# Kernel tuning notes

Hardware: AMD Instinct MI355X
Metric: run time of the kernel (lower is better)

## Reference

```python
import jax, jax.numpy as jnp
import numpy as np

B, N, D = 4, 2048, 1024

def setup_inputs() -> dict:
    key = jax.random.key(0)
    ks = jax.random.split(key, 8)
    s = 1.0 / np.sqrt(D)
    return {
        "x": jax.random.normal(ks[0], (B, N, D), dtype=jnp.float32),
        "Wq": jax.random.normal(ks[1], (D, D), dtype=jnp.float32) * s,
        "bq": jnp.zeros((D,), dtype=jnp.float32),
        "Wk": jax.random.normal(ks[2], (D, D), dtype=jnp.float32) * s,
        "bk": jnp.zeros((D,), dtype=jnp.float32),
        "Wv": jax.random.normal(ks[3], (D, D), dtype=jnp.float32) * s,
        "bv": jnp.zeros((D,), dtype=jnp.float32),
        "gamma": jnp.ones((1,), dtype=jnp.float32),
    }

def reference(x, Wq, bq, Wk, bk, Wv, bv, gamma):
    d = x.shape[-1]
    delta = 1.0 / jnp.sqrt(jnp.asarray(d, dtype=x.dtype))
    # torch Linear: y = x @ W.T + b, W is [out, in]
    Q = jnp.einsum('bnd,ed->bne', x, Wq) + bq
    K = jnp.einsum('bnd,ed->bne', x, Wk) + bk
    V = jnp.einsum('bnd,ed->bne', x, Wv) + bv
    scores = jnp.einsum('bne,bme->bnm', Q, K) * delta  # [B, N, N]
    attn = jax.nn.softmax(scores, axis=-1)
    out = jnp.einsum('bnm,bme->bne', attn, V)
    return out * gamma + x
```

## Files before the change

### kernel.cpp

```cpp
#include <hip/hip_runtime.h>

typedef _Float16 f16;
typedef __attribute__((ext_vector_type(4))) _Float16 f16x4;
typedef __attribute__((ext_vector_type(8))) _Float16 f16x8;
typedef __attribute__((ext_vector_type(4))) float f32x4;

#define B_ 4
#define N_ 2048
#define D_ 1024

#define FENCE asm volatile("" ::: "memory")

__global__ __launch_bounds__(256) void k_cast_all(const float4* __restrict__ x,
                                                  const float4* __restrict__ wq,
                                                  const float4* __restrict__ wk,
                                                  const float4* __restrict__ wv,
                                                  f16x4* __restrict__ xo,
                                                  f16x4* __restrict__ wqo,
                                                  f16x4* __restrict__ wko,
                                                  f16x4* __restrict__ wvo,
                                                  float* __restrict__ rowsum) {
  int b = blockIdx.x;
  if (b >= 11264) {
    rowsum[(b - 11264) * 256 + threadIdx.x] = 0.f;
    return;
  }
  const float4* in;
  f16x4* out;
  int idx;
  if (b < 8192)       { in = x;  out = xo;  idx = b * 256 + threadIdx.x; }
  else if (b < 9216)  { in = wq; out = wqo; idx = (b - 8192) * 256 + threadIdx.x; }
  else if (b < 10240) { in = wk; out = wko; idx = (b - 9216) * 256 + threadIdx.x; }
  else                { in = wv; out = wvo; idx = (b - 10240) * 256 + threadIdx.x; }
  float4 v = in[idx];
  f16x4 o = { (_Float16)v.x, (_Float16)v.y, (_Float16)v.z, (_Float16)v.w };
  out[idx] = o;
}

__device__ __forceinline__ void stage_half(const char* g0, int ldB, int kByte,
                                           char* slot, int tid) {
#pragma unroll
  for (int r = 0; r < 2; ++r) {
    int lin = r * 8192 + tid * 16;
    int row = lin >> 7;
    int lch = ((lin >> 4) & 7) ^ (row & 7);
    const char* g = g0 + (long)row * ldB + kByte + lch * 16;
    char* l = slot + r * 8192 + ((tid >> 6) << 10);
    __builtin_amdgcn_global_load_lds(
        (const __attribute__((address_space(1))) unsigned int*)g,
        (__attribute__((address_space(3))) unsigned int*)l, 16, 0, 0);
  }
}

#define RD_A(dst, base)                                                          \
  _Pragma("unroll") for (int i_ = 0; i_ < 4; ++i_) {                             \
    int rA_ = wm * 64 + i_ * 16 + l16;                                           \
    _Pragma("unroll") for (int k_ = 0; k_ < 2; ++k_)                             \
      dst[i_][k_] = *(const f16x8*)((base) + rA_ * 128 +                         \
                                    ((((k_ << 2) | quad) ^ l7) << 4));           \
  }
#define RD_B(dst, base)                                                          \
  _Pragma("unroll") for (int j_ = 0; j_ < 2; ++j_) {                             \
    int rB_ = wn * 32 + j_ * 16 + l16;                                           \
    _Pragma("unroll") for (int k_ = 0; k_ < 2; ++k_)                             \
      dst[j_][k_] = *(const f16x8*)((base) + rB_ * 128 +                         \
                                    ((((k_ << 2) | quad) ^ l7) << 4));           \
  }
#define MFMA8(Av, Bv, BH)                                                        \
  __builtin_amdgcn_s_setprio(1);                                                 \
  _Pragma("unroll") for (int i_ = 0; i_ < 4; ++i_)                               \
  _Pragma("unroll") for (int j_ = 0; j_ < 2; ++j_)                               \
  _Pragma("unroll") for (int k_ = 0; k_ < 2; ++k_)                               \
    acc[i_][BH][j_] = __builtin_amdgcn_mfma_f32_16x16x32_f16(                    \
        Av[i_][k_], Bv[j_][k_], acc[i_][BH][j_], 0, 0, 0);                       \
  __builtin_amdgcn_s_setprio(0);

#define D128_TILE(AC, B0C, AN, B0N, q) {                                         \
  char* Sc = lds + (q) * 49152;                                                  \
  char* Sn = lds + ((q) ^ 1) * 49152;                                            \
  const int kB = (t + 1) << 7;                                                   \
           \
  stage_half(gA, ldaB, kB, Sn, tid);                                             \
  stage_half(gB, ldbB, kB, Sn + 16384, tid);                                     \
  asm volatile("s_waitcnt vmcnt(4)" ::: "memory");                               \
  __builtin_amdgcn_s_barrier(); FENCE;                                           \
  RD_B(b1, Sc + 32768);                                                          \
  MFMA8(AC, B0C, 0);                                                             \
                         \
  stage_half(gB1, ldbB, kB, Sn + 32768, tid);                                    \
  asm volatile("s_waitcnt vmcnt(2)" ::: "memory");                               \
  __builtin_amdgcn_s_barrier(); FENCE;                                           \
  RD_A(AN, Sn); RD_B(B0N, Sn + 16384);                                           \
  MFMA8(AC, b1, 1);                                                              \
}
#define D128_TAIL(AC, B0C, q) {                                                  \
  char* Sc = lds + (q) * 49152;                                                  \
  asm volatile("s_waitcnt vmcnt(0)" ::: "memory");                               \
  __builtin_amdgcn_s_barrier(); FENCE;                                           \
  RD_B(b1, Sc + 32768);                                                          \
  MFMA8(AC, B0C, 0);                                                             \
  MFMA8(AC, b1, 1);                                                              \
}

__device__ __forceinline__ void gemm_d128(const char* gA, int ldaB,
                                          const char* gB, int ldbB,
                                          int nK, char* lds, f32x4 acc[4][2][2]) {
  const int tid = threadIdx.x;
  const int lane = tid & 63, wave = tid >> 6;
  const int wm = wave >> 2, wn = wave & 3;
  const int quad = lane >> 4, l16 = lane & 15;
  const int l7 = l16 & 7;
  const char* gB1 = gB + (long)128 * ldbB;
  f16x8 aX[4][2], aY[4][2], b0X[2][2], b0Y[2][2], b1[2][2];
  stage_half(gA,  ldaB, 0, lds, tid);
  stage_half(gB,  ldbB, 0, lds + 16384, tid);
  stage_half(gB1, ldbB, 0, lds + 32768, tid);
  asm volatile("s_waitcnt vmcnt(2)" ::: "memory");
  __builtin_amdgcn_s_barrier(); FENCE;
  RD_A(aX, lds); RD_B(b0X, lds + 16384);
  for (int tb = 0; tb < nK - 2; tb += 2) {
    { const int t = tb;     D128_TILE(aX, b0X, aY, b0Y, 0) }
    { const int t = tb + 1; D128_TILE(aY, b0Y, aX, b0X, 1) }
  }
  { const int t = nK - 2;   D128_TILE(aX, b0X, aY, b0Y, 0) }
  D128_TAIL(aY, b0Y, 1)
  __builtin_amdgcn_s_barrier(); FENCE;
}

__device__ __forceinline__ void gemm256(const char* gA, int ldaB,
                                        const char* gB, int ldbB,
                                        int nK, char* lds, f32x4 acc[2][4][2][2]) {
  const int tid = threadIdx.x;
  const int lane = tid & 63;
  const int wave = tid >> 6;
  const int wm = wave >> 2, wn = wave & 3;
  const int quad = lane >> 4, l16 = lane & 15;
  const int l7 = l16 & 7;
  const char* gA1 = gA + (long)128 * ldaB;
  const char* gB1 = gB + (long)128 * ldbB;
  char* Abuf = lds;
  char* Bbuf = lds + 65536;
  stage_half(gA,  ldaB, 0, Abuf, tid);
  stage_half(gB,  ldbB, 0, Bbuf, tid);
  stage_half(gA1, ldaB, 0, Abuf + 16384, tid);
  stage_half(gB1, ldbB, 0, Bbuf + 16384, tid);
  for (int t = 0; t < nK; ++t) {
    const int c = t & 1;
    char* Ac = Abuf + c * 32768;
    char* Bc = Bbuf + c * 32768;
    char* An = Abuf + (c ^ 1) * 32768;
    char* Bn = Bbuf + (c ^ 1) * 32768;
    const bool st = (t + 1 < nK);
    const int kB = (t + 1) << 7;
    f16x8 afc[2][4][2];
    f16x8 bf[2][2];
#pragma unroll
    for (int ph = 0; ph < 4; ++ph) {
      const int Ah = ph & 1, Bh = ph >> 1;
      if (ph == 0)      { asm volatile("s_waitcnt vmcnt(4)" ::: "memory"); }
      else if (ph == 1) { if (st) asm volatile("s_waitcnt vmcnt(4)" ::: "memory");
                          else    asm volatile("s_waitcnt vmcnt(2)" ::: "memory"); }
      else if (ph == 2) { if (st) asm volatile("s_waitcnt vmcnt(4)" ::: "memory");
                          else    asm volatile("s_waitcnt vmcnt(0)" ::: "memory"); }
      __builtin_amdgcn_s_barrier();
      FENCE;
      if (ph < 2) {
        const char* Ab = Ac + ph * 16384;
#pragma unroll
        for (int i = 0; i < 4; ++i) {
          int rA = wm * 64 + i * 16 + l16;
#pragma unroll
          for (int kk = 0; kk < 2; ++kk)
            afc[ph][i][kk] = *(const f16x8*)(Ab + rA * 128 + ((((kk << 2) | quad) ^ l7) << 4));
        }
      }
      if (Ah == 0) {
        const char* Bb = Bc + Bh * 16384;
#pragma unroll
        for (int jn = 0; jn < 2; ++jn) {
          int rB = wn * 32 + jn * 16 + l16;
#pragma unroll
          for (int kk = 0; kk < 2; ++kk)
            bf[jn][kk] = *(const f16x8*)(Bb + rB * 128 + ((((kk << 2) | quad) ^ l7) << 4));
        }
      }
      if (st) {
        if (ph == 0)      stage_half(gA,  ldaB, kB, An, tid);
        else if (ph == 1) stage_half(gB,  ldbB, kB, Bn, tid);
        else if (ph == 2) stage_half(gA1, ldaB, kB, An + 16384, tid);
        else              stage_half(gB1, ldbB, kB, Bn + 16384, tid);
      }
      FENCE;
      __builtin_amdgcn_s_barrier();
      __builtin_amdgcn_s_setprio(1);
#pragma unroll
      for (int i = 0; i < 4; ++i)
#pragma unroll
        for (int jn = 0; jn < 2; ++jn)
#pragma unroll
          for (int kk = 0; kk < 2; ++kk)
            acc[Ah][i][Bh][jn] = __builtin_amdgcn_mfma_f32_16x16x32_f16(
                afc[Ah][i][kk], bf[jn][kk], acc[Ah][i][Bh][jn], 0, 0, 0);
      __builtin_amdgcn_s_setprio(0);
    }
  }
  asm volatile("s_waitcnt vmcnt(0)" ::: "memory");
  __builtin_amdgcn_s_barrier();
  FENCE;
}

__global__ __launch_bounds__(512, 2) void k_qkv(const f16* __restrict__ X,
                                                const f16* __restrict__ Wq,
                                                const f16* __restrict__ Wk,
                                                const f16* __restrict__ Wv,
                                                const float* __restrict__ bq,
                                                const float* __restrict__ bk,
                                                const float* __restrict__ bv,
                                                f16* __restrict__ Q, f16* __restrict__ Ko,
                                                f16* __restrict__ Vt) {
  __shared__ __align__(16) char lds[98304];
  int fid = blockIdx.x;
  int xcd = fid & 7, k = fid >> 3;
  int rowt = xcd * 8 + (k & 7);
  int colt = k >> 3;
  int tm = rowt * 128;
  int w = colt >> 2;
  int tn = (colt & 3) * 256;
  const f16* Wsel = (w == 0) ? Wq : (w == 1) ? Wk : Wv;
  f32x4 acc[4][2][2];
#pragma unroll
  for (int i = 0; i < 4; ++i)
#pragma unroll
    for (int Bh = 0; Bh < 2; ++Bh)
#pragma unroll
      for (int jn = 0; jn < 2; ++jn) acc[i][Bh][jn] = (f32x4){0.f, 0.f, 0.f, 0.f};
  gemm_d128((const char*)(X + (long)tm * D_), D_ * 2,
            (const char*)(Wsel + (long)tn * D_), D_ * 2, D_ / 64, lds, acc);
  const int tid = threadIdx.x;
  const int lane = tid & 63, wave = tid >> 6;
  const int wm = wave >> 2, wn = wave & 3;
  const int quad = lane >> 4, l16 = lane & 15;
  if (w < 2) {
    const float* bias = w ? bk : bq;
    f16* outp = w ? Ko : Q;
#pragma unroll
    for (int Bh = 0; Bh < 2; ++Bh)
#pragma unroll
      for (int jn = 0; jn < 2; ++jn) {
        int col = tn + Bh * 128 + wn * 32 + jn * 16 + l16;
        float bb = bias[col];
#pragma unroll
        for (int i = 0; i < 4; ++i) {
          int rbase = tm + wm * 64 + i * 16 + quad * 4;
#pragma unroll
          for (int r = 0; r < 4; ++r)
            outp[(long)(rbase + r) * D_ + col] = (_Float16)(acc[i][Bh][jn][r] + bb);
        }
      }
  } else {
    int bidx = tm >> 11, ntok = tm & 2047;
    f16* VtB = Vt + (long)bidx * D_ * N_ + ntok;
    f16* ldsT = (f16*)lds;
#pragma unroll
    for (int Bh = 0; Bh < 2; ++Bh)
#pragma unroll
      for (int jn = 0; jn < 2; ++jn) {
        int fl = Bh * 128 + wn * 32 + jn * 16 + l16;
        float bb = bv[tn + fl];
#pragma unroll
        for (int i = 0; i < 4; ++i) {
          int rl = wm * 64 + i * 16 + quad * 4;
          f16x4 p = { (_Float16)(acc[i][Bh][jn][0] + bb), (_Float16)(acc[i][Bh][jn][1] + bb),
                      (_Float16)(acc[i][Bh][jn][2] + bb), (_Float16)(acc[i][Bh][jn][3] + bb) };
          *(f16x4*)(ldsT + fl * 136 + rl) = p;
        }
      }
    FENCE;
    __builtin_amdgcn_s_barrier();
    FENCE;
#pragma unroll
    for (int p = 0; p < 8; ++p) {
      int f = p * 32 + (tid >> 4);
      int cc = tid & 15;
      f16x8 v = *(const f16x8*)(ldsT + f * 136 + cc * 8);
      *(f16x8*)(VtB + (long)(tn + f) * N_ + cc * 8) = v;
    }
  }
}

__global__ __launch_bounds__(512, 2) void k_scores(const f16* __restrict__ Qf,
                                                   const f16* __restrict__ Kf,
                                                   f16* __restrict__ S,
                                                   float* __restrict__ rowsum) {
  __shared__ __align__(16) char lds[131072];
  int fid = blockIdx.x;
  int xcd = fid & 7, k = fid >> 3;
  int lin = xcd * 32 + k;
  int b = lin >> 6;
  int t = lin & 63;
  int rowt = t & 7, colt = t >> 3;
  int tm = rowt * 256, tn = colt * 256;
  f32x4 acc[2][4][2][2];
#pragma unroll
  for (int Ah = 0; Ah < 2; ++Ah)
#pragma unroll
    for (int i = 0; i < 4; ++i)
#pragma unroll
      for (int Bh = 0; Bh < 2; ++Bh)
#pragma unroll
        for (int jn = 0; jn < 2; ++jn) acc[Ah][i][Bh][jn] = (f32x4){0.f, 0.f, 0.f, 0.f};
  gemm256((const char*)(Qf + (long)b * N_ * D_ + (long)tm * D_), D_ * 2,
          (const char*)(Kf + (long)b * N_ * D_ + (long)tn * D_), D_ * 2,
          D_ / 64, lds, acc);
  const int tid = threadIdx.x;
  const int lane = tid & 63, wave = tid >> 6;
  const int wm = wave >> 2, wn = wave & 3;
  const int quad = lane >> 4, l16 = lane & 15;
  f16* Sb = S + (long)b * N_ * N_;
  const float delta = 0.03125f;
  f16* ldsS = (f16*)lds;
  float rsum[2][4][4];
#pragma unroll
  for (int Ah = 0; Ah < 2; ++Ah)
#pragma unroll
    for (int i = 0; i < 4; ++i)
#pragma unroll
      for (int r = 0; r < 4; ++r) rsum[Ah][i][r] = 0.f;
#pragma unroll
  for (int Bh = 0; Bh < 2; ++Bh) {
    FENCE;
    __builtin_amdgcn_s_barrier();
    FENCE;
#pragma unroll
    for (int Ah = 0; Ah < 2; ++Ah)
#pragma unroll
      for (int i = 0; i < 4; ++i) {
        int rloc = Ah * 128 + wm * 64 + i * 16 + quad * 4;
#pragma unroll
        for (int jn = 0; jn < 2; ++jn) {
          int col = wn * 32 + jn * 16 + l16;
#pragma unroll
          for (int r = 0; r < 4; ++r) {
            float e = __expf(acc[Ah][i][Bh][jn][r] * delta);
            rsum[Ah][i][r] += e;
            ldsS[(rloc + r) * 136 + col] = (_Float16)e;
          }
        }
      }
    FENCE;
    __builtin_amdgcn_s_barrier();
    FENCE;
#pragma unroll
    for (int p = 0; p < 8; ++p) {
      int row = p * 32 + (tid >> 4);
      int cc = tid & 15;
      f16x8 v = *(const f16x8*)(ldsS + row * 136 + cc * 8);
      *(f16x8*)(Sb + (long)(tm + row) * N_ + tn + Bh * 128 + cc * 8) = v;
    }
  }
#pragma unroll
  for (int m = 1; m < 16; m <<= 1)
#pragma unroll
    for (int Ah = 0; Ah < 2; ++Ah)
#pragma unroll
      for (int i = 0; i < 4; ++i)
#pragma unroll
        for (int r = 0; r < 4; ++r) rsum[Ah][i][r] += __shfl_xor(rsum[Ah][i][r], m);
  if (l16 == 0) {
    float* rs = rowsum + (long)b * N_ + tm;
#pragma unroll
    for (int Ah = 0; Ah < 2; ++Ah)
#pragma unroll
      for (int i = 0; i < 4; ++i)
#pragma unroll
        for (int r = 0; r < 4; ++r)
          atomicAdd(rs + Ah * 128 + wm * 64 + i * 16 + quad * 4 + r, rsum[Ah][i][r]);
  }
}

__global__ __launch_bounds__(512, 2) void k_out(const f16* __restrict__ P,
                                                const f16* __restrict__ Vt,
                                                const f16* __restrict__ xf,
                                                const float* __restrict__ gamma,
                                                const float* __restrict__ rowsum,
                                                float* __restrict__ out) {
  __shared__ __align__(16) char lds[98304];
  int fid = blockIdx.x;
  int xcd = fid & 7, kq = fid >> 3;
  int lin = xcd * 32 + kq;
  int b = lin >> 6;
  int t = lin & 63;
  int rowt = t >> 2, colt = t & 3;
  int tm = rowt * 128, tn = colt * 256;
  f32x4 acc[4][2][2];
#pragma unroll
  for (int i = 0; i < 4; ++i)
#pragma unroll
    for (int Bh = 0; Bh < 2; ++Bh)
#pragma unroll
      for (int jn = 0; jn < 2; ++jn) acc[i][Bh][jn] = (f32x4){0.f, 0.f, 0.f, 0.f};
  gemm_d128((const char*)(P + (long)b * N_ * N_ + (long)tm * N_), N_ * 2,
            (const char*)(Vt + (long)b * D_ * N_ + (long)tn * N_), N_ * 2,
            N_ / 64, lds, acc);
  const int tid = threadIdx.x;
  const int lane = tid & 63, wave = tid >> 6;
  const int wm = wave >> 2, wn = wave & 3;
  const int quad = lane >> 4, l16 = lane & 15;
  float g = gamma[0];
  float inv[4][4];
#pragma unroll
  for (int i = 0; i < 4; ++i)
#pragma unroll
    for (int r = 0; r < 4; ++r)
      inv[i][r] = g / rowsum[(long)b * N_ + tm + wm * 64 + i * 16 + quad * 4 + r];
#pragma unroll
  for (int Bh = 0; Bh < 2; ++Bh)
#pragma unroll
    for (int jn = 0; jn < 2; ++jn) {
      int col = tn + Bh * 128 + wn * 32 + jn * 16 + l16;
#pragma unroll
      for (int i = 0; i < 4; ++i) {
        int rbase = tm + wm * 64 + i * 16 + quad * 4;
#pragma unroll
        for (int r = 0; r < 4; ++r) {
          long idx = (long)b * N_ * D_ + (long)(rbase + r) * D_ + col;
          out[idx] = acc[i][Bh][jn][r] * inv[i][r] + (float)xf[idx];
        }
      }
    }
}

extern "C" void kernel_launch(void* const* d_in, const int* in_sizes, int n_in,
                              void* d_out, int out_size, void* d_ws, size_t ws_size,
                              hipStream_t stream) {
  const float* x  = (const float*)d_in[0];
  const float* Wq = (const float*)d_in[1];
  const float* bq = (const float*)d_in[2];
  const float* Wk = (const float*)d_in[3];
  const float* bk = (const float*)d_in[4];
  const float* Wv = (const float*)d_in[5];
  const float* bv = (const float*)d_in[6];
  const float* gamma = (const float*)d_in[7];
  float* out = (float*)d_out;
  char* ws = (char*)d_ws;

  f16* Qb  = (f16*)(ws);
  f16* Kb  = (f16*)(ws + (16u << 20));
  f16* Vt  = (f16*)(ws + (32u << 20));
  f16* Xb  = (f16*)(ws + (48u << 20));
  f16* Wqb = (f16*)(ws + (64u << 20));
  f16* Wkb = (f16*)(ws + (66u << 20));
  f16* Wvb = (f16*)(ws + (68u << 20));
  f16* S   = (f16*)(ws + (64u << 20));
  float* rowsum = (float*)(ws + (96u << 20));

  k_cast_all<<<11296, 256, 0, stream>>>((const float4*)x, (const float4*)Wq,
                                        (const float4*)Wk, (const float4*)Wv,
                                        (f16x4*)Xb, (f16x4*)Wqb, (f16x4*)Wkb, (f16x4*)Wvb,
                                        rowsum);
  k_qkv<<<768, 512, 0, stream>>>(Xb, Wqb, Wkb, Wvb, bq, bk, bv, Qb, Kb, Vt);
  k_scores<<<256, 512, 0, stream>>>(Qb, Kb, S, rowsum);
  k_out<<<256, 512, 0, stream>>>(S, Vt, Xb, gamma, rowsum, out);
}
```

Before: 238.6 us.

## Use 256x256 tiles for QKV projection and re-pipeline gemm256 with register prefetch

The QKV projection moves from 128x256 tiles (768 blocks) to 256x256 tiles (384 blocks) using gemm256. gemm256 is rewritten to prefetch LDS fragments into double-buffered registers, so MFMA work overlaps with the next fragment reads, and global staging is spread across the phases. The V transpose epilogue now runs in two passes through a 256-wide LDS buffer. Bigger tiles raise arithmetic intensity and cut redundant global reads. The costs are 128KB of LDS per block, more registers, and 384 blocks, which may not fill all CUs evenly. The rewritten gemm256 is also used by k_scores, so that kernel's pipeline changes too.

```diff
diff --git a/kernel.cpp b/kernel.cpp
--- a/kernel.cpp
+++ b/kernel.cpp
@@ -74,19 +74,78 @@
     acc[i_][BH][j_] = __builtin_amdgcn_mfma_f32_16x16x32_f16(                    \
         Av[i_][k_], Bv[j_][k_], acc[i_][BH][j_], 0, 0, 0);                       \
   __builtin_amdgcn_s_setprio(0);
+#define MFMA16(Av, Bv, AH, BH)                                                   \
+  __builtin_amdgcn_s_setprio(1);                                                 \
+  _Pragma("unroll") for (int i_ = 0; i_ < 4; ++i_)                               \
+  _Pragma("unroll") for (int j_ = 0; j_ < 2; ++j_)                               \
+  _Pragma("unroll") for (int k_ = 0; k_ < 2; ++k_)                               \
+    acc[AH][i_][BH][j_] = __builtin_amdgcn_mfma_f32_16x16x32_f16(                \
+        Av[i_][k_], Bv[j_][k_], acc[AH][i_][BH][j_], 0, 0, 0);                   \
+  __builtin_amdgcn_s_setprio(0);
+
+__device__ __forceinline__ void gemm256(const char* gA, int ldaB,
+                                        const char* gB, int ldbB,
+                                        int nK, char* lds, f32x4 acc[2][4][2][2]) {
+  const int tid = threadIdx.x;
+  const int lane = tid & 63, wave = tid >> 6;
+  const int wm = wave >> 2, wn = wave & 3;
+  const int quad = lane >> 4, l16 = lane & 15;
+  const int l7 = l16 & 7;
+  const char* gA1 = gA + (long)128 * ldaB;
+  const char* gB1 = gB + (long)128 * ldbB;
+  char* Abuf = lds;
+  char* Bbuf = lds + 65536;
+  f16x8 a0[4][2], a1[4][2], bX[2][2], bY[2][2];
+  stage_half(gA,  ldaB, 0, Abuf, tid);
+  stage_half(gB,  ldbB, 0, Bbuf, tid);
+  stage_half(gA1, ldaB, 0, Abuf + 16384, tid);
+  stage_half(gB1, ldbB, 0, Bbuf + 16384, tid);
+  asm volatile("s_waitcnt vmcnt(4)" ::: "memory");
+  __builtin_amdgcn_s_barrier(); FENCE;
+  RD_A(a0, Abuf); RD_B(bX, Bbuf);
+  for (int t = 0; t < nK; ++t) {
+    const int c = t & 1;
+    char* Ac = Abuf + c * 32768;
+    char* Bc = Bbuf + c * 32768;
+    char* An = Abuf + (c ^ 1) * 32768;
+    char* Bn = Bbuf + (c ^ 1) * 32768;
+    const bool st = (t + 1 < nK);
+    const int kB = (t + 1) << 7;
+    if (st) { stage_half(gA, ldaB, kB, An, tid); stage_half(gB, ldbB, kB, Bn, tid); }
+    if (st) asm volatile("s_waitcnt vmcnt(6)" ::: "memory");
+    else    asm volatile("s_waitcnt vmcnt(2)" ::: "memory");
+    __builtin_amdgcn_s_barrier(); FENCE;
+    RD_A(a1, Ac + 16384);
+    MFMA16(a0, bX, 0, 0);
+    if (st) asm volatile("s_waitcnt vmcnt(4)" ::: "memory");
+    else    asm volatile("s_waitcnt vmcnt(0)" ::: "memory");
+    __builtin_amdgcn_s_barrier(); FENCE;
+    RD_B(bY, Bc + 16384);
+    MFMA16(a1, bX, 1, 0);
+    if (st) { stage_half(gA1, ldaB, kB, An + 16384, tid); stage_half(gB1, ldbB, kB, Bn + 16384, tid); }
+    if (st) asm volatile("s_waitcnt vmcnt(4)" ::: "memory");
+    __builtin_amdgcn_s_barrier(); FENCE;
+    if (st) RD_B(bX, Bn);
+    MFMA16(a0, bY, 0, 1);
+    __builtin_amdgcn_s_barrier(); FENCE;
+    if (st) RD_A(a0, An);
+    MFMA16(a1, bY, 1, 1);
+  }
+  asm volatile("s_waitcnt vmcnt(0)" ::: "memory");
+  __builtin_amdgcn_s_barrier();
+  FENCE;
+}
 
 #define D128_TILE(AC, B0C, AN, B0N, q) {                                         \
   char* Sc = lds + (q) * 49152;                                                  \
   char* Sn = lds + ((q) ^ 1) * 49152;                                            \
   const int kB = (t + 1) << 7;                                                   \
-           \
   stage_half(gA, ldaB, kB, Sn, tid);                                             \
   stage_half(gB, ldbB, kB, Sn + 16384, tid);                                     \
   asm volatile("s_waitcnt vmcnt(4)" ::: "memory");                               \
   __builtin_amdgcn_s_barrier(); FENCE;                                           \
   RD_B(b1, Sc + 32768);                                                          \
   MFMA8(AC, B0C, 0);                                                             \
-                         \
   stage_half(gB1, ldbB, kB, Sn + 32768, tid);                                    \
   asm volatile("s_waitcnt vmcnt(2)" ::: "memory");                               \
   __builtin_amdgcn_s_barrier(); FENCE;                                           \
@@ -127,88 +186,6 @@
   __builtin_amdgcn_s_barrier(); FENCE;
 }
 
-__device__ __forceinline__ void gemm256(const char* gA, int ldaB,
-                                        const char* gB, int ldbB,
-                                        int nK, char* lds, f32x4 acc[2][4][2][2]) {
-  const int tid = threadIdx.x;
-  const int lane = tid & 63;
-  const int wave = tid >> 6;
-  const int wm = wave >> 2, wn = wave & 3;
-  const int quad = lane >> 4, l16 = lane & 15;
-  const int l7 = l16 & 7;
-  const char* gA1 = gA + (long)128 * ldaB;
-  const char* gB1 = gB + (long)128 * ldbB;
-  char* Abuf = lds;
-  char* Bbuf = lds + 65536;
-  stage_half(gA,  ldaB, 0, Abuf, tid);
-  stage_half(gB,  ldbB, 0, Bbuf, tid);
-  stage_half(gA1, ldaB, 0, Abuf + 16384, tid);
-  stage_half(gB1, ldbB, 0, Bbuf + 16384, tid);
-  for (int t = 0; t < nK; ++t) {
-    const int c = t & 1;
-    char* Ac = Abuf + c * 32768;
-    char* Bc = Bbuf + c * 32768;
-    char* An = Abuf + (c ^ 1) * 32768;
-    char* Bn = Bbuf + (c ^ 1) * 32768;
-    const bool st = (t + 1 < nK);
-    const int kB = (t + 1) << 7;
-    f16x8 afc[2][4][2];
-    f16x8 bf[2][2];
-#pragma unroll
-    for (int ph = 0; ph < 4; ++ph) {
-      const int Ah = ph & 1, Bh = ph >> 1;
-      if (ph == 0)      { asm volatile("s_waitcnt vmcnt(4)" ::: "memory"); }
-      else if (ph == 1) { if (st) asm volatile("s_waitcnt vmcnt(4)" ::: "memory");
-                          else    asm volatile("s_waitcnt vmcnt(2)" ::: "memory"); }
-      else if (ph == 2) { if (st) asm volatile("s_waitcnt vmcnt(4)" ::: "memory");
-                          else    asm volatile("s_waitcnt vmcnt(0)" ::: "memory"); }
-      __builtin_amdgcn_s_barrier();
-      FENCE;
-      if (ph < 2) {
-        const char* Ab = Ac + ph * 16384;
-#pragma unroll
-        for (int i = 0; i < 4; ++i) {
-          int rA = wm * 64 + i * 16 + l16;
-#pragma unroll
-          for (int kk = 0; kk < 2; ++kk)
-            afc[ph][i][kk] = *(const f16x8*)(Ab + rA * 128 + ((((kk << 2) | quad) ^ l7) << 4));
-        }
-      }
-      if (Ah == 0) {
-        const char* Bb = Bc + Bh * 16384;
-#pragma unroll
-        for (int jn = 0; jn < 2; ++jn) {
-          int rB = wn * 32 + jn * 16 + l16;
-#pragma unroll
-          for (int kk = 0; kk < 2; ++kk)
-            bf[jn][kk] = *(const f16x8*)(Bb + rB * 128 + ((((kk << 2) | quad) ^ l7) << 4));
-        }
-      }
-      if (st) {
-        if (ph == 0)      stage_half(gA,  ldaB, kB, An, tid);
-        else if (ph == 1) stage_half(gB,  ldbB, kB, Bn, tid);
-        else if (ph == 2) stage_half(gA1, ldaB, kB, An + 16384, tid);
-        else              stage_half(gB1, ldbB, kB, Bn + 16384, tid);
-      }
-      FENCE;
-      __builtin_amdgcn_s_barrier();
-      __builtin_amdgcn_s_setprio(1);
-#pragma unroll
-      for (int i = 0; i < 4; ++i)
-#pragma unroll
-        for (int jn = 0; jn < 2; ++jn)
-#pragma unroll
-          for (int kk = 0; kk < 2; ++kk)
-            acc[Ah][i][Bh][jn] = __builtin_amdgcn_mfma_f32_16x16x32_f16(
-                afc[Ah][i][kk], bf[jn][kk], acc[Ah][i][Bh][jn], 0, 0, 0);
-      __builtin_amdgcn_s_setprio(0);
-    }
-  }
-  asm volatile("s_waitcnt vmcnt(0)" ::: "memory");
-  __builtin_amdgcn_s_barrier();
-  FENCE;
-}
-
 __global__ __launch_bounds__(512, 2) void k_qkv(const f16* __restrict__ X,
                                                 const f16* __restrict__ Wq,
                                                 const f16* __restrict__ Wk,
@@ -218,24 +195,26 @@
                                                 const float* __restrict__ bv,
                                                 f16* __restrict__ Q, f16* __restrict__ Ko,
                                                 f16* __restrict__ Vt) {
-  __shared__ __align__(16) char lds[98304];
+  __shared__ __align__(16) char lds[131072];
   int fid = blockIdx.x;
   int xcd = fid & 7, k = fid >> 3;
-  int rowt = xcd * 8 + (k & 7);
-  int colt = k >> 3;
-  int tm = rowt * 128;
+  int rowt = xcd * 4 + (k & 3);
+  int colt = k >> 2;
+  int tm = rowt * 256;
   int w = colt >> 2;
   int tn = (colt & 3) * 256;
   const f16* Wsel = (w == 0) ? Wq : (w == 1) ? Wk : Wv;
-  f32x4 acc[4][2][2];
-#pragma unroll
-  for (int i = 0; i < 4; ++i)
-#pragma unroll
-    for (int Bh = 0; Bh < 2; ++Bh)
-#pragma unroll
-      for (int jn = 0; jn < 2; ++jn) acc[i][Bh][jn] = (f32x4){0.f, 0.f, 0.f, 0.f};
-  gemm_d128((const char*)(X + (long)tm * D_), D_ * 2,
-            (const char*)(Wsel + (long)tn * D_), D_ * 2, D_ / 64, lds, acc);
+  f32x4 acc[2][4][2][2];
+#pragma unroll
+  for (int Ah = 0; Ah < 2; ++Ah)
+#pragma unroll
+    for (int i = 0; i < 4; ++i)
+#pragma unroll
+      for (int Bh = 0; Bh < 2; ++Bh)
+#pragma unroll
+        for (int jn = 0; jn < 2; ++jn) acc[Ah][i][Bh][jn] = (f32x4){0.f, 0.f, 0.f, 0.f};
+  gemm256((const char*)(X + (long)tm * D_), D_ * 2,
+          (const char*)(Wsel + (long)tn * D_), D_ * 2, D_ / 64, lds, acc);
   const int tid = threadIdx.x;
   const int lane = tid & 63, wave = tid >> 6;
   const int wm = wave >> 2, wn = wave & 3;
@@ -250,40 +229,50 @@
         int col = tn + Bh * 128 + wn * 32 + jn * 16 + l16;
         float bb = bias[col];
 #pragma unroll
-        for (int i = 0; i < 4; ++i) {
-          int rbase = tm + wm * 64 + i * 16 + quad * 4;
-#pragma unroll
-          for (int r = 0; r < 4; ++r)
-            outp[(long)(rbase + r) * D_ + col] = (_Float16)(acc[i][Bh][jn][r] + bb);
-        }
+        for (int Ah = 0; Ah < 2; ++Ah)
+#pragma unroll
+          for (int i = 0; i < 4; ++i) {
+            int rbase = tm + Ah * 128 + wm * 64 + i * 16 + quad * 4;
+#pragma unroll
+            for (int r = 0; r < 4; ++r)
+              outp[(long)(rbase + r) * D_ + col] = (_Float16)(acc[Ah][i][Bh][jn][r] + bb);
+          }
       }
   } else {
     int bidx = tm >> 11, ntok = tm & 2047;
     f16* VtB = Vt + (long)bidx * D_ * N_ + ntok;
     f16* ldsT = (f16*)lds;
 #pragma unroll
-    for (int Bh = 0; Bh < 2; ++Bh)
+    for (int pass = 0; pass < 2; ++pass) {
+      FENCE;
+      __builtin_amdgcn_s_barrier();
+      FENCE;
 #pragma unroll
       for (int jn = 0; jn < 2; ++jn) {
-        int fl = Bh * 128 + wn * 32 + jn * 16 + l16;
-        float bb = bv[tn + fl];
-#pragma unroll
-        for (int i = 0; i < 4; ++i) {
-          int rl = wm * 64 + i * 16 + quad * 4;
-          f16x4 p = { (_Float16)(acc[i][Bh][jn][0] + bb), (_Float16)(acc[i][Bh][jn][1] + bb),
-                      (_Float16)(acc[i][Bh][jn][2] + bb), (_Float16)(acc[i][Bh][jn][3] + bb) };
-          *(f16x4*)(ldsT + fl * 136 + rl) = p;
-        }
+        int fl = wn * 32 + jn * 16 + l16;
+        float bb = bv[tn + pass * 128 + fl];
+#pragma unroll
+        for (int Ah = 0; Ah < 2; ++Ah)
+#pragma unroll
+          for (int i = 0; i < 4; ++i) {
+            int rl = Ah * 128 + wm * 64 + i * 16 + quad * 4;
+            f16x4 p = { (_Float16)(acc[Ah][i][pass][jn][0] + bb),
+                        (_Float16)(acc[Ah][i][pass][jn][1] + bb),
+                        (_Float16)(acc[Ah][i][pass][jn][2] + bb),
+                        (_Float16)(acc[Ah][i][pass][jn][3] + bb) };
+            *(f16x4*)(ldsT + fl * 264 + rl) = p;
+          }
       }
-    FENCE;
-    __builtin_amdgcn_s_barrier();
-    FENCE;
-#pragma unroll
-    for (int p = 0; p < 8; ++p) {
-      int f = p * 32 + (tid >> 4);
-      int cc = tid & 15;
-      f16x8 v = *(const f16x8*)(ldsT + f * 136 + cc * 8);
-      *(f16x8*)(VtB + (long)(tn + f) * N_ + cc * 8) = v;
+      FENCE;
+      __builtin_amdgcn_s_barrier();
+      FENCE;
+#pragma unroll
+      for (int p = 0; p < 8; ++p) {
+        int f = p * 16 + (tid >> 5);
+        int cc = tid & 31;
+        f16x8 v = *(const f16x8*)(ldsT + f * 264 + cc * 8);
+        *(f16x8*)(VtB + (long)(tn + pass * 128 + f) * N_ + cc * 8) = v;
+      }
     }
   }
 }
@@ -458,7 +447,7 @@
                                         (const float4*)Wk, (const float4*)Wv,
                                         (f16x4*)Xb, (f16x4*)Wqb, (f16x4*)Wkb, (f16x4*)Wvb,
                                         rowsum);
-  k_qkv<<<768, 512, 0, stream>>>(Xb, Wqb, Wkb, Wvb, bq, bk, bv, Qb, Kb, Vt);
+  k_qkv<<<384, 512, 0, stream>>>(Xb, Wqb, Wkb, Wvb, bq, bk, bv, Qb, Kb, Vt);
   k_scores<<<256, 512, 0, stream>>>(Qb, Kb, S, rowsum);
   k_out<<<256, 512, 0, stream>>>(S, Vt, Xb, gamma, rowsum, out);
 }
```

Result: no change. 235.6 us (-1.3%).
